# Performance work log

Measured on AMD Instinct MI355X. Metric: run time of the kernel, lower is better.

Reference implementation:

```python
import jax, jax.numpy as jnp
import numpy as np
from jax import lax

B, T, D = 16384, 60, 36   # n_traj, n_tp, n_dims
L, C, S = 10, 20, 9       # latent_dim, cluster_num, n_static
OUT = 8                   # mlp out (use_static=False)


def setup_inputs() -> dict:
    key = jax.random.key(0)
    ks = jax.random.split(key, 12)

    def w(k, shape):
        return jax.random.normal(k, shape, jnp.float32) / np.float32(np.sqrt(shape[0]))

    return {
        "data": jax.random.normal(ks[0], (B, T, D), jnp.float32),
        "time_steps": jnp.arange(T, dtype=jnp.float32),
        "static_data": jax.random.normal(ks[1], (B, S), jnp.float32),
        # GRU_unit_cluster gates: Linear(latent_dim + input_dim -> latent_dim)
        "W_update": w(ks[2], (L + D, L)), "b_update": jnp.zeros((L,), jnp.float32),
        "W_reset": w(ks[3], (L + D, L)), "b_reset": jnp.zeros((L,), jnp.float32),
        "W_new": w(ks[4], (L + D, L)), "b_new": jnp.zeros((L,), jnp.float32),
        # infer_emitter_z: Linear(latent_dim + cluster_num -> cluster_num)
        "W_emit": w(ks[5], (L + C, C)), "b_emit": jnp.zeros((C,), jnp.float32),
        # stand-in ODE func (z0_diffeq_solver.ode_func): tanh(Linear(latent->latent))
        "W_ode": w(ks[6], (L, L)), "b_ode": jnp.zeros((L,), jnp.float32),
        # final mlp: Linear(ts*10 + static -> 8)
        "W_mlp": w(ks[7], (T * L + S, OUT)), "b_mlp": jnp.zeros((OUT,), jnp.float32),
    }


def _forward(data, time_steps, static_data,
             W_update, b_update, W_reset, b_reset, W_new, b_new,
             W_emit, b_emit, W_ode, b_ode, W_mlp, b_mlp):
    n_traj = data.shape[0]
    # per-step dt: first step uses the synthetic 0.01 offset, then consecutive diffs
    dts = jnp.concatenate([jnp.full((1,), 0.01, time_steps.dtype), jnp.diff(time_steps)])
    xs = jnp.swapaxes(data, 0, 1)  # [T, B, D]

    def step(carry, inp):
        y_state, y_prob = carry        # [B, L], [B, C]
        x_t, dt = inp                  # [B, D], scalar
        # Euler step of the ODE between observations
        yi_ode = y_state + jnp.tanh(y_state @ W_ode + b_ode) * dt
        # GRU_unit_cluster update
        yc = jnp.concatenate([yi_ode, x_t], axis=-1)          # [B, L+D]
        u = jax.nn.sigmoid(yc @ W_update + b_update)
        r = jax.nn.sigmoid(yc @ W_reset + b_reset)
        cc = jnp.concatenate([yi_ode * r, x_t], axis=-1)
        new = cc @ W_new + b_new
        y_new = (1.0 - u) * new + u * yi_ode                  # [B, L]
        # emit_probs (concat_data=True path)
        zin = jnp.concatenate([y_prob, y_new], axis=-1)       # [B, C+L]
        y_prob_new = jax.nn.softmax(zin @ W_emit + b_emit, axis=-1)
        return (y_new, y_prob_new), y_new

    init = (jnp.zeros((n_traj, L), data.dtype), jnp.zeros((n_traj, C), data.dtype))
    _, states = lax.scan(step, init, (xs, dts))               # states: [T, B, L]

    vec = jnp.swapaxes(states, 0, 1).reshape(n_traj, T * L)   # [B, T*L]
    vec = jnp.concatenate([vec, static_data], axis=-1)        # [B, T*L + S]
    return vec @ W_mlp + b_mlp                                # [B, 8]


def reference(data, time_steps, static_data,
              W_update, b_update, W_reset, b_reset, W_new, b_new,
              W_emit, b_emit, W_ode, b_ode, W_mlp, b_mlp):
    return _forward(data, time_steps, static_data,
                    W_update, b_update, W_reset, b_reset, W_new, b_new,
                    W_emit, b_emit, W_ode, b_ode, W_mlp, b_mlp)
```

## Files before the change

### kernel.cpp

```cpp
#include <hip/hip_runtime.h>
#include <hip/hip_fp16.h>
#include <math.h>

#define B_TRAJ 16384
#define T_STEPS 60
#define D_IN 36
#define L_DIM 10
#define C_NUM 20
#define S_STAT 9
#define OUT_DIM 8
#define TT 2
#define NTILE (T_STEPS / TT)

__device__ __forceinline__ float rcp_fast(float x) { return __builtin_amdgcn_rcpf(x); }
__device__ __forceinline__ float sigm_fast(float x) { return rcp_fast(1.0f + __expf(-x)); }
__device__ __forceinline__ float tanh_fast(float x) {
    x = fminf(fmaxf(x, -10.0f), 10.0f);
    float e = __expf(2.0f * x);
    return (e - 1.0f) * rcp_fast(e + 1.0f);
}
#define WFENCE() __builtin_amdgcn_wave_barrier()

__global__ __launch_bounds__(256) __attribute__((amdgpu_waves_per_eu(4, 8)))
void dgm2_v5(
    const float* __restrict__ data,
    const float* __restrict__ time_steps,
    const float* __restrict__ static_data,
    const float* __restrict__ W_update,
    const float* __restrict__ b_update,
    const float* __restrict__ W_reset,
    const float* __restrict__ b_reset,
    const float* __restrict__ W_new,
    const float* __restrict__ b_new,
    const float* __restrict__ W_emit,
    const float* __restrict__ b_emit,
    const float* __restrict__ W_ode,
    const float* __restrict__ b_ode,
    const float* __restrict__ W_mlp,
    const float* __restrict__ b_mlp,
    float* __restrict__ out)
{
    __shared__ __align__(16) __half xprojH[8][61][32];
    __shared__ __align__(16) float WGX[D_IN][32];
    __shared__ __align__(16) float wbuf[4][292];
    __shared__ float dts[T_STEPS];

    const int tid  = threadIdx.x;
    const int w    = tid >> 6;
    const int lane = tid & 63;
    const int half = lane >> 5;
    const int s    = lane & 31;
    const int ltraj = w * 2 + half;
    const int traj  = blockIdx.x * 8 + ltraj;

    for (int i = tid; i < D_IN * 30; i += 256) {
        const int k = i / 30, c = i % 30;
        float v;
        if (c < 10)      v = W_update[(L_DIM + k) * L_DIM + c];
        else if (c < 20) v = W_reset [(L_DIM + k) * L_DIM + (c - 10)];
        else             v = W_new   [(L_DIM + k) * L_DIM + (c - 20)];
        WGX[k][c] = v;
    }
    for (int i = tid; i < D_IN * 2; i += 256) WGX[i >> 1][30 + (i & 1)] = 0.0f;
    if (tid < T_STEPS) dts[tid] = (tid == 0) ? 0.01f : time_steps[tid] - time_steps[tid - 1];
    __syncthreads();

    {
        float wxp[D_IN];
#pragma unroll
        for (int k = 0; k < D_IN; ++k) wxp[k] = WGX[k][s];

        float* xst = &wbuf[w][0];
        const float* tbase = data + (size_t)(blockIdx.x * 8 + w * 2) * (T_STEPS * D_IN);
        const int sh  = lane / 18;
        const int sr  = lane % 18;
        const int stt = sr / 9;
        const int sc  = sr % 9;
        const bool stg = (lane < 36);

        if (stg) {
            const float4 v = *reinterpret_cast<const float4*>(
                tbase + (size_t)sh * (T_STEPS * D_IN) + stt * D_IN + sc * 4);
            *reinterpret_cast<float4*>(xst + ((0 * 2 + sh) * TT + stt) * 36 + sc * 4) = v;
        }
        WFENCE();

        for (int tile = 0; tile < NTILE; ++tile) {
            const int cb = tile & 1, nb = cb ^ 1;
            float4 pf = make_float4(0.f, 0.f, 0.f, 0.f);
            if (stg && (tile + 1 < NTILE)) {
                pf = *reinterpret_cast<const float4*>(
                    tbase + (size_t)sh * (T_STEPS * D_IN) + ((tile + 1) * TT + stt) * D_IN + sc * 4);
            }
#pragma unroll
            for (int tt = 0; tt < TT; ++tt) {
                const float* xrow = xst + ((cb * 2 + half) * TT + tt) * 36;
                float acc = 0.0f;
#pragma unroll
                for (int c = 0; c < 9; ++c) {
                    const float4 x4 = *reinterpret_cast<const float4*>(xrow + c * 4);
                    acc += x4.x * wxp[c * 4]     + x4.y * wxp[c * 4 + 1]
                         + x4.z * wxp[c * 4 + 2] + x4.w * wxp[c * 4 + 3];
                }
                if (s < 30) xprojH[ltraj][tile * TT + tt][s] = __float2half(acc);
            }
            if (stg && (tile + 1 < NTILE)) {
                *reinterpret_cast<float4*>(xst + ((nb * 2 + sh) * TT + stt) * 36 + sc * 4) = pf;
            }
            WFENCE();
        }
    }

    const bool uo = (s < 10);
    const bool ro = (s >= 10 && s < 20);
    const bool no = (s >= 20 && s < 30);
    const bool eo = (s >= 10 && s < 30);
    const int  gcol = uo ? s : (ro ? (s - 10) : (no ? (s - 20) : 0));

    const float* Wg = uo ? W_update : (ro ? W_reset : W_new);
    float wgy[L_DIM];
#pragma unroll
    for (int k = 0; k < L_DIM; ++k) wgy[k] = (s < 30) ? Wg[k * L_DIM + gcol] : 0.0f;

    float waux[30];
#pragma unroll
    for (int k = 0; k < 30; ++k) {
        float v = 0.0f;
        if (eo) v = W_emit[k * C_NUM + (s - 10)];
        else if (uo && k < L_DIM) v = W_ode[k * L_DIM + s];
        waux[k] = v;
    }
    const float bg    = uo ? b_update[s] : (ro ? b_reset[gcol] : (no ? b_new[gcol] : 0.0f));
    const float bode  = uo ? b_ode[s] : 0.0f;
    const float bemit = eo ? b_emit[s - 10] : 0.0f;

    float* bcYI = &wbuf[w][0]  + half * 12;
    float* bcR  = &wbuf[w][24] + half * 12;
    float* bcN  = &wbuf[w][48] + half * 12;
    float* bcY  = &wbuf[w][72] + half * 12;
    float* bcP  = &wbuf[w][96] + half * 20;

    float y[L_DIM];
#pragma unroll
    for (int k = 0; k < L_DIM; ++k) y[k] = 0.0f;
    float yown = 0.0f;
    if (eo) bcP[s - 10] = 0.0f;
    WFENCE();

    for (int t = 0; t < T_STEPS; ++t) {
        const float dt = dts[t];

        float g = bode;
#pragma unroll
        for (int k = 0; k < L_DIM; ++k) g += y[k] * waux[k];
        const float yis = fmaf(tanh_fast(g), dt, yown);
        if (uo) bcYI[s] = yis;
        WFENCE();
        {
            const float4 a = *reinterpret_cast<const float4*>(bcYI);
            const float4 b = *reinterpret_cast<const float4*>(bcYI + 4);
            const float2 c = *reinterpret_cast<const float2*>(bcYI + 8);
            y[0] = a.x; y[1] = a.y; y[2] = a.z; y[3] = a.w;
            y[4] = b.x; y[5] = b.y; y[6] = b.z; y[7] = b.w;
            y[8] = c.x; y[9] = c.y;
        }

        const float xa = __half2float(xprojH[ltraj][t][s]);
        const float accB = bg + xa;
        float accY = 0.0f;
#pragma unroll
        for (int k = 0; k < L_DIM; ++k) accY += y[k] * wgy[k];
        const float uval = sigm_fast(accB + accY);
        if (ro) bcR[s - 10] = uval;
        WFENCE();

        float accN = accB;
        {
            const float4 a = *reinterpret_cast<const float4*>(bcR);
            const float4 b = *reinterpret_cast<const float4*>(bcR + 4);
            const float2 c = *reinterpret_cast<const float2*>(bcR + 8);
            const float rv[L_DIM] = {a.x, a.y, a.z, a.w, b.x, b.y, b.z, b.w, c.x, c.y};
#pragma unroll
            for (int k = 0; k < L_DIM; ++k) accN += (y[k] * rv[k]) * wgy[k];
        }
        if (no) bcN[s - 20] = accN;
        WFENCE();

        if (uo) {
            const float nv = bcN[s];
            const float yn = fmaf(uval, yis - nv, nv);
            yown = yn;
            bcY[s] = yn;
            xprojH[ltraj][t][s] = __float2half(yn);
        }
        WFENCE();
        {
            const float4 a = *reinterpret_cast<const float4*>(bcY);
            const float4 b = *reinterpret_cast<const float4*>(bcY + 4);
            const float2 c = *reinterpret_cast<const float2*>(bcY + 8);
            y[0] = a.x; y[1] = a.y; y[2] = a.z; y[3] = a.w;
            y[4] = b.x; y[5] = b.y; y[6] = b.z; y[7] = b.w;
            y[8] = c.x; y[9] = c.y;
        }

        float zdot = 0.0f, zsum = 0.0f;
#pragma unroll
        for (int q = 0; q < 5; ++q) {
            const float4 z4 = *reinterpret_cast<const float4*>(bcP + q * 4);
            zdot += z4.x * waux[q * 4]     + z4.y * waux[q * 4 + 1]
                  + z4.z * waux[q * 4 + 2] + z4.w * waux[q * 4 + 3];
            zsum += (z4.x + z4.y) + (z4.z + z4.w);
        }
        const float pinv = (t == 0) ? 0.0f : rcp_fast(zsum);
        float ev = fmaf(zdot, pinv, bemit);
#pragma unroll
        for (int k = 0; k < L_DIM; ++k) ev += y[k] * waux[20 + k];
        const float zv = __expf(fminf(ev, 60.0f));
        if (eo) bcP[s - 10] = zv;
        WFENCE();
    }

    WFENCE();
    {
        const int g = s >> 3, col = s & 7;
        float o8 = 0.0f;
        for (int tb = 0; tb < 15; ++tb) {
            const int t = g + tb * 4;
            const __half2* yh = reinterpret_cast<const __half2*>(&xprojH[ltraj][t][0]);
            const float* wrow = W_mlp + (size_t)t * L_DIM * OUT_DIM + col;
#pragma unroll
            for (int q = 0; q < 5; ++q) {
                const float2 yv = __half22float2(yh[q]);
                o8 += yv.x * wrow[(2 * q) * OUT_DIM] + yv.y * wrow[(2 * q + 1) * OUT_DIM];
            }
        }
        o8 += __shfl_xor(o8, 8, 32);
        o8 += __shfl_xor(o8, 16, 32);
        if (s < OUT_DIM) {
            const float* stp = static_data + (size_t)traj * S_STAT;
            const float* wms = W_mlp + (size_t)(T_STEPS * L_DIM) * OUT_DIM;
#pragma unroll
            for (int i = 0; i < S_STAT; ++i) o8 += stp[i] * wms[i * OUT_DIM + s];
            out[(size_t)traj * OUT_DIM + s] = o8 + b_mlp[s];
        }
    }
}

extern "C" void kernel_launch(void* const* d_in, const int* in_sizes, int n_in,
                              void* d_out, int out_size, void* d_ws, size_t ws_size,
                              hipStream_t stream) {
    const float* data        = (const float*)d_in[0];
    const float* time_steps  = (const float*)d_in[1];
    const float* static_data = (const float*)d_in[2];
    const float* W_update    = (const float*)d_in[3];
    const float* b_update    = (const float*)d_in[4];
    const float* W_reset     = (const float*)d_in[5];
    const float* b_reset     = (const float*)d_in[6];
    const float* W_new       = (const float*)d_in[7];
    const float* b_new       = (const float*)d_in[8];
    const float* W_emit      = (const float*)d_in[9];
    const float* b_emit      = (const float*)d_in[10];
    const float* W_ode       = (const float*)d_in[11];
    const float* b_ode       = (const float*)d_in[12];
    const float* W_mlp       = (const float*)d_in[13];
    const float* b_mlp       = (const float*)d_in[14];
    float* out = (float*)d_out;

    dim3 grid(B_TRAJ / 8), block(256);
    hipLaunchKernelGGL(dgm2_v5, grid, block, 0, stream,
                       data, time_steps, static_data,
                       W_update, b_update, W_reset, b_reset, W_new, b_new,
                       W_emit, b_emit, W_ode, b_ode, W_mlp, b_mlp, out);
}
```

Before: 343.6 us.

## Replace LDS broadcast round-trips with bpermute/swizzle and fold biases into input projection

Restructures the per-step GRU recurrence. The reset-gated state is exchanged via ds_bpermute and the candidate value is routed back to the update lanes with bpermute, which removes one LDS broadcast stage. The softmax normalizer is computed with a ds_swizzle reduction instead of a serial sum plus reciprocal on the next step. Gate biases are folded into the precomputed half-precision x projection, exp/tanh/sigmoid use exp2 intrinsics, wave barriers become sched_barriers, and the time loop is unrolled by two. The wider per-wave scratch layout assumes wbuf has at least 256 floats per wave, and storing biases in half precision adds a small rounding error.

```diff
diff --git a/kernel.cpp b/kernel.cpp
--- a/kernel.cpp
+++ b/kernel.cpp
@@ -12,17 +12,21 @@
 #define TT 2
 #define NTILE (T_STEPS / TT)
 
+#define LOG2E 1.4426950408889634f
+
 __device__ __forceinline__ float rcp_fast(float x) { return __builtin_amdgcn_rcpf(x); }
-__device__ __forceinline__ float sigm_fast(float x) { return rcp_fast(1.0f + __expf(-x)); }
+__device__ __forceinline__ float exp2_fast(float x) { return __builtin_amdgcn_exp2f(x); }
+__device__ __forceinline__ float sigm_fast(float x) {
+    return rcp_fast(1.0f + exp2_fast(x * -LOG2E));
+}
 __device__ __forceinline__ float tanh_fast(float x) {
-    x = fminf(fmaxf(x, -10.0f), 10.0f);
-    float e = __expf(2.0f * x);
-    return (e - 1.0f) * rcp_fast(e + 1.0f);
-}
-#define WFENCE() __builtin_amdgcn_wave_barrier()
+    const float t = fminf(fmaxf(x * (2.0f * LOG2E), -30.0f), 30.0f);
+    return fmaf(-2.0f, rcp_fast(exp2_fast(t) + 1.0f), 1.0f);
+}
+#define SBAR() __builtin_amdgcn_sched_barrier(0x7F)
 
 __global__ __launch_bounds__(256) __attribute__((amdgpu_waves_per_eu(4, 8)))
-void dgm2_v5(
+void dgm2_v6(
     const float* __restrict__ data,
     const float* __restrict__ time_steps,
     const float* __restrict__ static_data,
@@ -65,6 +69,11 @@
     if (tid < T_STEPS) dts[tid] = (tid == 0) ? 0.01f : time_steps[tid] - time_steps[tid - 1];
     __syncthreads();
 
+    float bcol = 0.0f;
+    if (s < 10)      bcol = b_update[s];
+    else if (s < 20) bcol = b_reset[s - 10];
+    else if (s < 30) bcol = b_new[s - 20];
+
     {
         float wxp[D_IN];
 #pragma unroll
@@ -83,7 +92,7 @@
                 tbase + (size_t)sh * (T_STEPS * D_IN) + stt * D_IN + sc * 4);
             *reinterpret_cast<float4*>(xst + ((0 * 2 + sh) * TT + stt) * 36 + sc * 4) = v;
         }
-        WFENCE();
+        SBAR();
 
         for (int tile = 0; tile < NTILE; ++tile) {
             const int cb = tile & 1, nb = cb ^ 1;
@@ -95,19 +104,19 @@
 #pragma unroll
             for (int tt = 0; tt < TT; ++tt) {
                 const float* xrow = xst + ((cb * 2 + half) * TT + tt) * 36;
-                float acc = 0.0f;
+                float acc = bcol;
 #pragma unroll
                 for (int c = 0; c < 9; ++c) {
                     const float4 x4 = *reinterpret_cast<const float4*>(xrow + c * 4);
                     acc += x4.x * wxp[c * 4]     + x4.y * wxp[c * 4 + 1]
                          + x4.z * wxp[c * 4 + 2] + x4.w * wxp[c * 4 + 3];
                 }
-                if (s < 30) xprojH[ltraj][tile * TT + tt][s] = __float2half(acc);
+                xprojH[ltraj][tile * TT + tt][s] = __float2half(acc);
             }
             if (stg && (tile + 1 < NTILE)) {
                 *reinterpret_cast<float4*>(xst + ((nb * 2 + sh) * TT + stt) * 36 + sc * 4) = pf;
             }
-            WFENCE();
+            SBAR();
         }
     }
 
@@ -130,23 +139,28 @@
         else if (uo && k < L_DIM) v = W_ode[k * L_DIM + s];
         waux[k] = v;
     }
-    const float bg    = uo ? b_update[s] : (ro ? b_reset[gcol] : (no ? b_new[gcol] : 0.0f));
     const float bode  = uo ? b_ode[s] : 0.0f;
     const float bemit = eo ? b_emit[s - 10] : 0.0f;
 
-    float* bcYI = &wbuf[w][0]  + half * 12;
-    float* bcR  = &wbuf[w][24] + half * 12;
-    float* bcN  = &wbuf[w][48] + half * 12;
-    float* bcY  = &wbuf[w][72] + half * 12;
-    float* bcP  = &wbuf[w][96] + half * 20;
+    const int lanebase = half << 5;
+    const int slotB = (s - 10) & 31;
+    const int nperm = (lanebase + (uo ? s + 20 : s)) << 2;
+    const int rperm = (lanebase + ((s - 10) & 31)) << 2;
+
+    float* wb   = &wbuf[w][0];
+    float* bcYI = wb       + lanebase;
+    float* bcR  = wb + 64  + lanebase;
+    float* bcY  = wb + 128 + lanebase;
+    float* bcP  = wb + 192 + lanebase;
 
     float y[L_DIM];
 #pragma unroll
     for (int k = 0; k < L_DIM; ++k) y[k] = 0.0f;
     float yown = 0.0f;
-    if (eo) bcP[s - 10] = 0.0f;
-    WFENCE();
-
+    bcP[slotB] = 0.0f;
+    SBAR();
+
+#pragma unroll 2
     for (int t = 0; t < T_STEPS; ++t) {
         const float dt = dts[t];
 
@@ -154,8 +168,8 @@
 #pragma unroll
         for (int k = 0; k < L_DIM; ++k) g += y[k] * waux[k];
         const float yis = fmaf(tanh_fast(g), dt, yown);
-        if (uo) bcYI[s] = yis;
-        WFENCE();
+        bcYI[s] = yis;
+        SBAR();
         {
             const float4 a = *reinterpret_cast<const float4*>(bcYI);
             const float4 b = *reinterpret_cast<const float4*>(bcYI + 4);
@@ -164,36 +178,35 @@
             y[4] = b.x; y[5] = b.y; y[6] = b.z; y[7] = b.w;
             y[8] = c.x; y[9] = c.y;
         }
+        const float yi_r = __int_as_float(__builtin_amdgcn_ds_bpermute(rperm, __float_as_int(yis)));
 
         const float xa = __half2float(xprojH[ltraj][t][s]);
-        const float accB = bg + xa;
-        float accY = 0.0f;
+        float accY = xa;
 #pragma unroll
         for (int k = 0; k < L_DIM; ++k) accY += y[k] * wgy[k];
-        const float uval = sigm_fast(accB + accY);
-        if (ro) bcR[s - 10] = uval;
-        WFENCE();
-
-        float accN = accB;
-        {
-            const float4 a = *reinterpret_cast<const float4*>(bcR);
-            const float4 b = *reinterpret_cast<const float4*>(bcR + 4);
-            const float2 c = *reinterpret_cast<const float2*>(bcR + 8);
-            const float rv[L_DIM] = {a.x, a.y, a.z, a.w, b.x, b.y, b.z, b.w, c.x, c.y};
-#pragma unroll
-            for (int k = 0; k < L_DIM; ++k) accN += (y[k] * rv[k]) * wgy[k];
-        }
-        if (no) bcN[s - 20] = accN;
-        WFENCE();
-
-        if (uo) {
-            const float nv = bcN[s];
-            const float yn = fmaf(uval, yis - nv, nv);
-            yown = yn;
-            bcY[s] = yn;
-            xprojH[ltraj][t][s] = __float2half(yn);
-        }
-        WFENCE();
+        const float uval = sigm_fast(accY);
+        bcR[s] = uval * yi_r;
+        SBAR();
+
+        float accN = xa;
+        {
+            const float4 a = *reinterpret_cast<const float4*>(bcR + 10 - 10);
+        }
+        {
+            const float2 p0 = *reinterpret_cast<const float2*>(bcR + 10);
+            const float4 p1 = *reinterpret_cast<const float4*>(bcR + 12);
+            const float4 p2 = *reinterpret_cast<const float4*>(bcR + 16);
+            const float rv[L_DIM] = {p0.x, p0.y, p1.x, p1.y, p1.z, p1.w, p2.x, p2.y, p2.z, p2.w};
+#pragma unroll
+            for (int k = 0; k < L_DIM; ++k) accN += rv[k] * wgy[k];
+        }
+        const float nv = __int_as_float(__builtin_amdgcn_ds_bpermute(nperm, __float_as_int(accN)));
+
+        const float yn = fmaf(uval, yis - nv, nv);
+        yown = yn;
+        bcY[s] = yn;
+        xprojH[ltraj][t][s] = __float2half(yn);
+        SBAR();
         {
             const float4 a = *reinterpret_cast<const float4*>(bcY);
             const float4 b = *reinterpret_cast<const float4*>(bcY + 4);
@@ -203,24 +216,28 @@
             y[8] = c.x; y[9] = c.y;
         }
 
-        float zdot = 0.0f, zsum = 0.0f;
+        float ev = bemit;
 #pragma unroll
         for (int q = 0; q < 5; ++q) {
             const float4 z4 = *reinterpret_cast<const float4*>(bcP + q * 4);
-            zdot += z4.x * waux[q * 4]     + z4.y * waux[q * 4 + 1]
-                  + z4.z * waux[q * 4 + 2] + z4.w * waux[q * 4 + 3];
-            zsum += (z4.x + z4.y) + (z4.z + z4.w);
-        }
-        const float pinv = (t == 0) ? 0.0f : rcp_fast(zsum);
-        float ev = fmaf(zdot, pinv, bemit);
+            ev += z4.x * waux[q * 4]     + z4.y * waux[q * 4 + 1]
+                + z4.z * waux[q * 4 + 2] + z4.w * waux[q * 4 + 3];
+        }
 #pragma unroll
         for (int k = 0; k < L_DIM; ++k) ev += y[k] * waux[20 + k];
-        const float zv = __expf(fminf(ev, 60.0f));
-        if (eo) bcP[s - 10] = zv;
-        WFENCE();
-    }
-
-    WFENCE();
+        const float zv = exp2_fast(fminf(ev * LOG2E, 86.0f));
+
+        float zs = eo ? zv : 0.0f;
+        zs += __int_as_float(__builtin_amdgcn_ds_swizzle(__float_as_int(zs), 0x041F));
+        zs += __int_as_float(__builtin_amdgcn_ds_swizzle(__float_as_int(zs), 0x081F));
+        zs += __int_as_float(__builtin_amdgcn_ds_swizzle(__float_as_int(zs), 0x101F));
+        zs += __int_as_float(__builtin_amdgcn_ds_swizzle(__float_as_int(zs), 0x201F));
+        zs += __int_as_float(__builtin_amdgcn_ds_swizzle(__float_as_int(zs), 0x401F));
+        bcP[slotB] = zv * rcp_fast(zs);
+        SBAR();
+    }
+
+    SBAR();
     {
         const int g = s >> 3, col = s & 7;
         float o8 = 0.0f;
@@ -267,7 +284,7 @@
     float* out = (float*)d_out;
 
     dim3 grid(B_TRAJ / 8), block(256);
-    hipLaunchKernelGGL(dgm2_v5, grid, block, 0, stream,
+    hipLaunchKernelGGL(dgm2_v6, grid, block, 0, stream,
                        data, time_steps, static_data,
                        W_update, b_update, W_reset, b_reset, W_new, b_new,
                        W_emit, b_emit, W_ode, b_ode, W_mlp, b_mlp, out);
```

Measured after the change: 361.6 us. +5.2%, slower.
